# Kernel tuning notes

Hardware: AMD Instinct MI355X
Metric: run time of the kernel (lower is better)

## Reference

```python
import jax, jax.numpy as jnp
import numpy as np

# 47 skeleton edges (parent, child) from getSkeletalModelStructure()
EDGES = np.array([
    (0, 1), (1, 2), (2, 3), (3, 29), (1, 5), (5, 6), (6, 8), (8, 9), (8, 13),
    (8, 17), (8, 21), (8, 25), (9, 10), (10, 11), (11, 12), (13, 14), (14, 15),
    (15, 16), (17, 18), (18, 19), (19, 20), (21, 22), (22, 23), (23, 24),
    (25, 26), (26, 27), (27, 28), (29, 30), (29, 34), (29, 38), (29, 42),
    (29, 46), (30, 31), (31, 32), (32, 33), (34, 35), (35, 36), (36, 37),
    (38, 39), (39, 40), (40, 41), (42, 43), (43, 44), (44, 45), (46, 47),
    (47, 48), (48, 49)], dtype=np.int32)

N_JOINTS = 50
N_EDGES = 47


def _length_direct(pose):
    # pose: [B, T, 151]; drop counter channel, view as joints
    B, T = pose.shape[0], pose.shape[1]
    p = pose[..., :-1].reshape(B, T, N_JOINTS, 3)
    diff = p[:, :, EDGES[:, 0], :] - p[:, :, EDGES[:, 1], :]   # [B, T, 47, 3]
    length = jnp.linalg.norm(diff, axis=-1)                      # [B, T, 47]
    eps = jnp.finfo(pose.dtype).tiny
    direct = diff / (length + eps)[..., None]                    # [B, T, 47, 3]
    # torch stacks each [B,T,3] edge dir along dim=-1 -> [B,T,3,47], then reshapes
    directs = jnp.transpose(direct, (0, 1, 3, 2)).reshape(B, T, N_EDGES * 3)
    return length, directs


def setup_inputs() -> dict:
    key = jax.random.key(0)
    k1, k2 = jax.random.split(key)
    B, T, D = 128, 1024, 151
    preds = jax.random.normal(k1, (B, T, D), dtype=jnp.float32)
    targets = jax.random.normal(k2, (B, T, D), dtype=jnp.float32)
    return {"preds": preds, "targets": targets}


def reference(preds, targets):
    target_pad = 0.0
    mask = (targets != target_pad).astype(preds.dtype)           # [B, T, 151]
    preds_m = preds * mask
    targets_m = targets * mask
    _, preds_dir = _length_direct(preds_m)
    _, targets_dir = _length_direct(targets_m)
    preds_dir = preds_dir * mask[:, :, :N_EDGES * 3]
    targets_dir = targets_dir * mask[:, :, :N_EDGES * 3]
    # cfg: loss='l1' (mean abs), vel_loss='mse' (mean square), loss_scale=1.0
    l1 = jnp.mean(jnp.abs(preds_m - targets_m))
    vel_mse = jnp.mean(jnp.square(preds_dir - targets_dir))
    return l1 + 0.1 * vel_mse
```

## Files before the change

### kernel.cpp

```cpp
#include <hip/hip_runtime.h>


#define N_ROWS   (128 * 1024)
#define ROW      151
#define N_EDGES  47
#define GRID     8192
#define BLOCK    256
#define ROWS_PER_WAVE 4
#define WAVE_DWORDS (ROWS_PER_WAVE * ROW)
#define WAVE_F4 (WAVE_DWORDS / 4)
#define WAVE_TASKS (ROWS_PER_WAVE * N_EDGES)
#define S_STRIDE (ROW * 2)

#if __has_builtin(__builtin_amdgcn_rsqf)
__device__ __forceinline__ float fast_rsq(float x) { return __builtin_amdgcn_rsqf(x); }
#else
__device__ __forceinline__ float fast_rsq(float x) {
    float r; asm volatile("v_rsq_f32 %0, %1" : "=v"(r) : "v"(x)); return r;
}
#endif

#define E(p, c) ((unsigned)((p) * 6) | ((unsigned)((c) * 6) << 16))
__constant__ unsigned c_edge[N_EDGES] = {
    E(0,1),  E(1,2),  E(2,3),  E(3,29), E(1,5),  E(5,6),  E(6,8),  E(8,9),
    E(8,13), E(8,17), E(8,21), E(8,25), E(9,10), E(10,11),E(11,12),E(13,14),
    E(14,15),E(15,16),E(17,18),E(18,19),E(19,20),E(21,22),E(22,23),E(23,24),
    E(25,26),E(26,27),E(27,28),E(29,30),E(29,34),E(29,38),E(29,42),E(29,46),
    E(30,31),E(31,32),E(32,33),E(34,35),E(35,36),E(36,37),E(38,39),E(39,40),
    E(40,41),E(42,43),E(43,44),E(44,45),E(46,47),E(47,48),E(48,49)};

__global__ __launch_bounds__(BLOCK) void reg_loss_main(
        const float* __restrict__ preds, const float* __restrict__ targets,
        float* __restrict__ wsL, float* __restrict__ wsV) {
    __shared__ float S[4][ROWS_PER_WAVE * S_STRIDE];
    __shared__ float redL[4], redV[4];

    const int t = threadIdx.x;
    const int lane = t & 63;
    const int wave = t >> 6;
    float* __restrict__ Sw = S[wave];
    float4* __restrict__ S4 = (float4*)Sw;

    const long long base = ((long long)blockIdx.x * 4 + wave) * WAVE_DWORDS;
    const float4* __restrict__ p4 = (const float4*)(preds + base);
    const float4* __restrict__ t4 = (const float4*)(targets + base);

    int tr[3], te[3], tpi[3], tci[3];
#pragma unroll
    for (int k = 0; k < 3; ++k) {
        int task = lane + k * 64;
        int r = task / N_EDGES;
        int e = task - r * N_EDGES;
        if (task >= WAVE_TASKS) { r = 0; e = 0; }
        tr[k] = r; te[k] = e;
        unsigned pk = c_edge[e];
        tpi[k] = pk & 0xffff;
        tci[k] = pk >> 16;
    }

    float l1 = 0.f;
    float vel = 0.f;

#pragma unroll
    for (int k = 0; k < 3; ++k) {
        int i = lane + k * 64;
        if (i < WAVE_F4) {
            float4 pv = p4[i];
            float4 tv = t4[i];
            float4 pm;
            pm.x = (tv.x != 0.f) ? pv.x : 0.f;
            pm.y = (tv.y != 0.f) ? pv.y : 0.f;
            pm.z = (tv.z != 0.f) ? pv.z : 0.f;
            pm.w = (tv.w != 0.f) ? pv.w : 0.f;
            l1 += fabsf(pm.x - tv.x) + fabsf(pm.y - tv.y)
                + fabsf(pm.z - tv.z) + fabsf(pm.w - tv.w);
            float4 a = {pm.x, tv.x, pm.y, tv.y};
            float4 b = {pm.z, tv.z, pm.w, tv.w};
            S4[i * 2]     = a;
            S4[i * 2 + 1] = b;
        }
    }

#pragma unroll
    for (int k = 0; k < 3; ++k) {
        int task = lane + k * 64;
        if (task < WAVE_TASKS) {
            const float* __restrict__ R = Sw + tr[k] * S_STRIDE;
            int pi = tpi[k], ci = tci[k], e = te[k];
            float2 px = *(const float2*)(R + pi);
            float2 py = *(const float2*)(R + pi + 2);
            float2 pz = *(const float2*)(R + pi + 4);
            float2 cx = *(const float2*)(R + ci);
            float2 cy = *(const float2*)(R + ci + 2);
            float2 cz = *(const float2*)(R + ci + 4);
            float pdx = px.x - cx.x, pdy = py.x - cy.x, pdz = pz.x - cz.x;
            float tdx = px.y - cx.y, tdy = py.y - cy.y, tdz = pz.y - cz.y;
            float pd2 = pdx * pdx + pdy * pdy + pdz * pdz;
            float td2 = tdx * tdx + tdy * tdy + tdz * tdz;
            float pinv = (pd2 > 0.f) ? fast_rsq(pd2) : 0.f;
            float tinv = (td2 > 0.f) ? fast_rsq(td2) : 0.f;
            float dx = pdx * pinv - tdx * tinv;
            float dy = pdy * pinv - tdy * tinv;
            float dz = pdz * pinv - tdz * tinv;
            float m0 = (R[e * 2 + 1]        != 0.f) ? 1.f : 0.f;
            float m1 = (R[(47 + e) * 2 + 1] != 0.f) ? 1.f : 0.f;
            float m2 = (R[(94 + e) * 2 + 1] != 0.f) ? 1.f : 0.f;
            vel += m0 * dx * dx + m1 * dy * dy + m2 * dz * dz;
        }
    }

#pragma unroll
    for (int off = 32; off > 0; off >>= 1) {
        l1  += __shfl_down(l1, off);
        vel += __shfl_down(vel, off);
    }
    if (lane == 0) { redL[wave] = l1; redV[wave] = vel; }
    __syncthreads();
    if (t == 0) {
        wsL[blockIdx.x] = redL[0] + redL[1] + redL[2] + redL[3];
        wsV[blockIdx.x] = redV[0] + redV[1] + redV[2] + redV[3];
    }
}

__global__ __launch_bounds__(BLOCK) void reg_loss_finalize(
        const float* __restrict__ wsL, const float* __restrict__ wsV,
        float* __restrict__ out) {
    __shared__ double rl[4], rv[4];
    const int t = threadIdx.x;
    const int lane = t & 63;
    const int wave = t >> 6;
    double L = 0.0, V = 0.0;
    for (int k = t; k < GRID; k += BLOCK) { L += wsL[k]; V += wsV[k]; }
#pragma unroll
    for (int off = 32; off > 0; off >>= 1) {
        L += __shfl_down(L, off);
        V += __shfl_down(V, off);
    }
    if (lane == 0) { rl[wave] = L; rv[wave] = V; }
    __syncthreads();
    if (t == 0) {
        double Ls = rl[0] + rl[1] + rl[2] + rl[3];
        double Vs = rv[0] + rv[1] + rv[2] + rv[3];
        out[0] = (float)(Ls / ((double)N_ROWS * 151.0)
                       + 0.1 * (Vs / ((double)N_ROWS * 141.0)));
    }
}

extern "C" void kernel_launch(void* const* d_in, const int* in_sizes, int n_in,
                              void* d_out, int out_size, void* d_ws, size_t ws_size,
                              hipStream_t stream) {
    const float* preds   = (const float*)d_in[0];
    const float* targets = (const float*)d_in[1];
    float* wsL = (float*)d_ws;
    float* wsV = wsL + GRID;
    float* out = (float*)d_out;

    reg_loss_main<<<GRID, BLOCK, 0, stream>>>(preds, targets, wsL, wsV);
    reg_loss_finalize<<<1, BLOCK, 0, stream>>>(wsL, wsV, out);
}
```

Measured before the change: 180.7 us.

## Process eight row-chunks per wave with register double-buffered prefetch

Each wave now loops over eight 4-row chunks instead of handling a single chunk, and the grid shrinks from 8192 to 1024 blocks. The next chunk's global loads are issued into registers before the current chunk is masked, staged to LDS and reduced, so memory latency overlaps with compute. This amortizes the per-block reduction and launch cost and hides load latency. The trade-off is higher register pressure and fewer waves to saturate HBM bandwidth. The loop reuses the LDS buffer without any barrier, which is safe only because each wave stays in lockstep within its own region.

```diff
diff --git a/kernel.cpp b/kernel.cpp
--- a/kernel.cpp
+++ b/kernel.cpp
@@ -4,12 +4,13 @@
 #define N_ROWS   (128 * 1024)
 #define ROW      151
 #define N_EDGES  47
-#define GRID     8192
+#define GRID     1024
 #define BLOCK    256
-#define ROWS_PER_WAVE 4
-#define WAVE_DWORDS (ROWS_PER_WAVE * ROW)
-#define WAVE_F4 (WAVE_DWORDS / 4)
-#define WAVE_TASKS (ROWS_PER_WAVE * N_EDGES)
+#define WAVE_CHUNKS 8
+#define CHUNK_ROWS 4
+#define CHUNK_DWORDS (CHUNK_ROWS * ROW)
+#define CHUNK_F4 (CHUNK_DWORDS / 4)
+#define CHUNK_TASKS (CHUNK_ROWS * N_EDGES)
 #define S_STRIDE (ROW * 2)
 
 #if __has_builtin(__builtin_amdgcn_rsqf)
@@ -32,7 +33,7 @@
 __global__ __launch_bounds__(BLOCK) void reg_loss_main(
         const float* __restrict__ preds, const float* __restrict__ targets,
         float* __restrict__ wsL, float* __restrict__ wsV) {
-    __shared__ float S[4][ROWS_PER_WAVE * S_STRIDE];
+    __shared__ float S[4][CHUNK_ROWS * S_STRIDE];
     __shared__ float redL[4], redV[4];
 
     const int t = threadIdx.x;
@@ -41,71 +42,97 @@
     float* __restrict__ Sw = S[wave];
     float4* __restrict__ S4 = (float4*)Sw;
 
-    const long long base = ((long long)blockIdx.x * 4 + wave) * WAVE_DWORDS;
-    const float4* __restrict__ p4 = (const float4*)(preds + base);
-    const float4* __restrict__ t4 = (const float4*)(targets + base);
+    const long long wbase =
+        ((long long)blockIdx.x * 4 + wave) * (WAVE_CHUNKS * CHUNK_DWORDS);
+    const float4* __restrict__ p4 = (const float4*)(preds + wbase);
+    const float4* __restrict__ t4 = (const float4*)(targets + wbase);
 
-    int tr[3], te[3], tpi[3], tci[3];
+    int tRoff[3], tpi[3], tci[3], tm0[3];
+    bool tact[3];
 #pragma unroll
     for (int k = 0; k < 3; ++k) {
         int task = lane + k * 64;
+        tact[k] = task < CHUNK_TASKS;
         int r = task / N_EDGES;
         int e = task - r * N_EDGES;
-        if (task >= WAVE_TASKS) { r = 0; e = 0; }
-        tr[k] = r; te[k] = e;
+        if (!tact[k]) { r = 0; e = 0; }
+        tRoff[k] = r * S_STRIDE;
         unsigned pk = c_edge[e];
         tpi[k] = pk & 0xffff;
         tci[k] = pk >> 16;
+        tm0[k] = e * 2 + 1;
     }
 
     float l1 = 0.f;
     float vel = 0.f;
 
+    float4 Pp[3], Pt[3];
 #pragma unroll
     for (int k = 0; k < 3; ++k) {
         int i = lane + k * 64;
-        if (i < WAVE_F4) {
-            float4 pv = p4[i];
-            float4 tv = t4[i];
-            float4 pm;
-            pm.x = (tv.x != 0.f) ? pv.x : 0.f;
-            pm.y = (tv.y != 0.f) ? pv.y : 0.f;
-            pm.z = (tv.z != 0.f) ? pv.z : 0.f;
-            pm.w = (tv.w != 0.f) ? pv.w : 0.f;
-            l1 += fabsf(pm.x - tv.x) + fabsf(pm.y - tv.y)
-                + fabsf(pm.z - tv.z) + fabsf(pm.w - tv.w);
-            float4 a = {pm.x, tv.x, pm.y, tv.y};
-            float4 b = {pm.z, tv.z, pm.w, tv.w};
-            S4[i * 2]     = a;
-            S4[i * 2 + 1] = b;
-        }
+        if (i < CHUNK_F4) { Pp[k] = p4[i]; Pt[k] = t4[i]; }
     }
 
 #pragma unroll
-    for (int k = 0; k < 3; ++k) {
-        int task = lane + k * 64;
-        if (task < WAVE_TASKS) {
-            const float* __restrict__ R = Sw + tr[k] * S_STRIDE;
-            int pi = tpi[k], ci = tci[k], e = te[k];
-            float2 px = *(const float2*)(R + pi);
-            float2 py = *(const float2*)(R + pi + 2);
-            float2 pz = *(const float2*)(R + pi + 4);
-            float2 cx = *(const float2*)(R + ci);
-            float2 cy = *(const float2*)(R + ci + 2);
-            float2 cz = *(const float2*)(R + ci + 4);
-            float pdx = px.x - cx.x, pdy = py.x - cy.x, pdz = pz.x - cz.x;
-            float tdx = px.y - cx.y, tdy = py.y - cy.y, tdz = pz.y - cz.y;
-            float pd2 = pdx * pdx + pdy * pdy + pdz * pdz;
-            float td2 = tdx * tdx + tdy * tdy + tdz * tdz;
-            float pinv = (pd2 > 0.f) ? fast_rsq(pd2) : 0.f;
-            float tinv = (td2 > 0.f) ? fast_rsq(td2) : 0.f;
-            float dx = pdx * pinv - tdx * tinv;
-            float dy = pdy * pinv - tdy * tinv;
-            float dz = pdz * pinv - tdz * tinv;
-            float m0 = (R[e * 2 + 1]        != 0.f) ? 1.f : 0.f;
-            float m1 = (R[(47 + e) * 2 + 1] != 0.f) ? 1.f : 0.f;
-            float m2 = (R[(94 + e) * 2 + 1] != 0.f) ? 1.f : 0.f;
-            vel += m0 * dx * dx + m1 * dy * dy + m2 * dz * dz;
+    for (int c = 0; c < WAVE_CHUNKS; ++c) {
+        float4 Cp[3], Ct[3];
+#pragma unroll
+        for (int k = 0; k < 3; ++k) { Cp[k] = Pp[k]; Ct[k] = Pt[k]; }
+
+        if (c + 1 < WAVE_CHUNKS) {
+            const float4* np4 = p4 + (long long)(c + 1) * CHUNK_F4;
+            const float4* nt4 = t4 + (long long)(c + 1) * CHUNK_F4;
+#pragma unroll
+            for (int k = 0; k < 3; ++k) {
+                int i = lane + k * 64;
+                if (i < CHUNK_F4) { Pp[k] = np4[i]; Pt[k] = nt4[i]; }
+            }
+        }
+
+#pragma unroll
+        for (int k = 0; k < 3; ++k) {
+            int i = lane + k * 64;
+            if (i < CHUNK_F4) {
+                float4 pv = Cp[k], tv = Ct[k];
+                float4 pm;
+                pm.x = (tv.x != 0.f) ? pv.x : 0.f;
+                pm.y = (tv.y != 0.f) ? pv.y : 0.f;
+                pm.z = (tv.z != 0.f) ? pv.z : 0.f;
+                pm.w = (tv.w != 0.f) ? pv.w : 0.f;
+                l1 += fabsf(pm.x - tv.x) + fabsf(pm.y - tv.y)
+                    + fabsf(pm.z - tv.z) + fabsf(pm.w - tv.w);
+                float4 a = {pm.x, tv.x, pm.y, tv.y};
+                float4 b = {pm.z, tv.z, pm.w, tv.w};
+                S4[i * 2]     = a;
+                S4[i * 2 + 1] = b;
+            }
+        }
+
+#pragma unroll
+        for (int k = 0; k < 3; ++k) {
+            if (tact[k]) {
+                const float* __restrict__ R = Sw + tRoff[k];
+                int pi = tpi[k], ci = tci[k], me = tm0[k];
+                float2 px = *(const float2*)(R + pi);
+                float2 py = *(const float2*)(R + pi + 2);
+                float2 pz = *(const float2*)(R + pi + 4);
+                float2 cx = *(const float2*)(R + ci);
+                float2 cy = *(const float2*)(R + ci + 2);
+                float2 cz = *(const float2*)(R + ci + 4);
+                float pdx = px.x - cx.x, pdy = py.x - cy.x, pdz = pz.x - cz.x;
+                float tdx = px.y - cx.y, tdy = py.y - cy.y, tdz = pz.y - cz.y;
+                float pd2 = pdx * pdx + pdy * pdy + pdz * pdz;
+                float td2 = tdx * tdx + tdy * tdy + tdz * tdz;
+                float pinv = (pd2 > 0.f) ? fast_rsq(pd2) : 0.f;
+                float tinv = (td2 > 0.f) ? fast_rsq(td2) : 0.f;
+                float dx = pdx * pinv - tdx * tinv;
+                float dy = pdy * pinv - tdy * tinv;
+                float dz = pdz * pinv - tdz * tinv;
+                float m0 = (R[me]       != 0.f) ? 1.f : 0.f;
+                float m1 = (R[me + 94]  != 0.f) ? 1.f : 0.f;
+                float m2 = (R[me + 188] != 0.f) ? 1.f : 0.f;
+                vel += m0 * dx * dx + m1 * dy * dy + m2 * dz * dz;
+            }
         }
     }
 
```

New measurement: 179.8 us. Within noise of the previous version (-0.5%).

## Double-buffer per-wave chunks via global_load_lds DMA with fewer, longer-lived blocks

Applied to the files above, without the earlier changes.

Each wave now handles four 4-row chunks instead of one. Chunks are loaded straight into LDS through global_load_lds into two alternating buffers, and manual vmcnt/lgkmcnt waits overlap the next chunk's load with the current chunk's compute. The staged layout is no longer interleaved: preds and targets sit in separate LDS regions, and masking is recomputed from the targets during the edge pass. The grid shrinks 4x, so there are fewer waves to hide latency, and correctness depends on the hand-counted waitcnt values.

```diff
diff --git a/kernel.cpp b/kernel.cpp
--- a/kernel.cpp
+++ b/kernel.cpp
@@ -4,13 +4,13 @@
 #define N_ROWS   (128 * 1024)
 #define ROW      151
 #define N_EDGES  47
-#define GRID     8192
+#define GRID     2048
 #define BLOCK    256
-#define ROWS_PER_WAVE 4
-#define WAVE_DWORDS (ROWS_PER_WAVE * ROW)
-#define WAVE_F4 (WAVE_DWORDS / 4)
-#define WAVE_TASKS (ROWS_PER_WAVE * N_EDGES)
-#define S_STRIDE (ROW * 2)
+#define CHUNKS   4
+#define CHUNK_ROWS 4
+#define CHUNK_DW (CHUNK_ROWS * ROW)
+#define CHUNK_TASKS (CHUNK_ROWS * N_EDGES)
+#define BUF_DW (2 * CHUNK_DW)
 
 #if __has_builtin(__builtin_amdgcn_rsqf)
 __device__ __forceinline__ float fast_rsq(float x) { return __builtin_amdgcn_rsqf(x); }
@@ -20,7 +20,34 @@
 }
 #endif
 
-#define E(p, c) ((unsigned)((p) * 6) | ((unsigned)((c) * 6) << 16))
+template <int N>
+__device__ __forceinline__ void wait_vm() {
+    asm volatile("s_waitcnt vmcnt(%0)" :: "n"(N) : "memory");
+}
+__device__ __forceinline__ void wait_lgkm0() {
+    asm volatile("s_waitcnt lgkmcnt(0)" ::: "memory");
+}
+
+__device__ __forceinline__ void dma16(const float* g, float* l) {
+    __builtin_amdgcn_global_load_lds(
+        (const __attribute__((address_space(1))) unsigned*)g,
+        (__attribute__((address_space(3))) unsigned*)l, 16, 0, 0);
+}
+
+__device__ __forceinline__ void dma_chunk(const float* gp, const float* gt,
+                                          float* L, int lane) {
+    const int l4 = lane * 4;
+    dma16(gp + l4,        L);
+    dma16(gp + 256 + l4,  L + 256);
+    dma16(gt + l4,        L + CHUNK_DW);
+    dma16(gt + 256 + l4,  L + CHUNK_DW + 256);
+    if (lane < 23) {
+        dma16(gp + 512 + l4, L + 512);
+        dma16(gt + 512 + l4, L + CHUNK_DW + 512);
+    }
+}
+
+#define E(p, c) ((unsigned)((p) * 3) | ((unsigned)((c) * 3) << 16))
 __constant__ unsigned c_edge[N_EDGES] = {
     E(0,1),  E(1,2),  E(2,3),  E(3,29), E(1,5),  E(5,6),  E(6,8),  E(8,9),
     E(8,13), E(8,17), E(8,21), E(8,25), E(9,10), E(10,11),E(11,12),E(13,14),
@@ -29,72 +56,47 @@
     E(30,31),E(31,32),E(32,33),E(34,35),E(35,36),E(36,37),E(38,39),E(39,40),
     E(40,41),E(42,43),E(43,44),E(44,45),E(46,47),E(47,48),E(48,49)};
 
-__global__ __launch_bounds__(BLOCK) void reg_loss_main(
-        const float* __restrict__ preds, const float* __restrict__ targets,
-        float* __restrict__ wsL, float* __restrict__ wsV) {
-    __shared__ float S[4][ROWS_PER_WAVE * S_STRIDE];
-    __shared__ float redL[4], redV[4];
-
-    const int t = threadIdx.x;
-    const int lane = t & 63;
-    const int wave = t >> 6;
-    float* __restrict__ Sw = S[wave];
-    float4* __restrict__ S4 = (float4*)Sw;
-
-    const long long base = ((long long)blockIdx.x * 4 + wave) * WAVE_DWORDS;
-    const float4* __restrict__ p4 = (const float4*)(preds + base);
-    const float4* __restrict__ t4 = (const float4*)(targets + base);
-
-    int tr[3], te[3], tpi[3], tci[3];
-#pragma unroll
-    for (int k = 0; k < 3; ++k) {
-        int task = lane + k * 64;
-        int r = task / N_EDGES;
-        int e = task - r * N_EDGES;
-        if (task >= WAVE_TASKS) { r = 0; e = 0; }
-        tr[k] = r; te[k] = e;
-        unsigned pk = c_edge[e];
-        tpi[k] = pk & 0xffff;
-        tci[k] = pk >> 16;
-    }
-
-    float l1 = 0.f;
-    float vel = 0.f;
+struct TaskDesc { int act[3], roff[3], pi[3], ci[3], me[3]; };
+
+__device__ __forceinline__ void compute_chunk(
+        const float* __restrict__ B, int lane, const TaskDesc& td,
+        float& l1, float& vel) {
+    const float* __restrict__ Bp = B;
+    const float* __restrict__ Bt = B + CHUNK_DW;
 
 #pragma unroll
     for (int k = 0; k < 3; ++k) {
         int i = lane + k * 64;
-        if (i < WAVE_F4) {
-            float4 pv = p4[i];
-            float4 tv = t4[i];
-            float4 pm;
-            pm.x = (tv.x != 0.f) ? pv.x : 0.f;
-            pm.y = (tv.y != 0.f) ? pv.y : 0.f;
-            pm.z = (tv.z != 0.f) ? pv.z : 0.f;
-            pm.w = (tv.w != 0.f) ? pv.w : 0.f;
-            l1 += fabsf(pm.x - tv.x) + fabsf(pm.y - tv.y)
-                + fabsf(pm.z - tv.z) + fabsf(pm.w - tv.w);
-            float4 a = {pm.x, tv.x, pm.y, tv.y};
-            float4 b = {pm.z, tv.z, pm.w, tv.w};
-            S4[i * 2]     = a;
-            S4[i * 2 + 1] = b;
+        if (i < CHUNK_DW / 4) {
+            float4 pv = ((const float4*)Bp)[i];
+            float4 tv = ((const float4*)Bt)[i];
+            float a0 = (tv.x != 0.f) ? pv.x : 0.f;
+            float a1 = (tv.y != 0.f) ? pv.y : 0.f;
+            float a2 = (tv.z != 0.f) ? pv.z : 0.f;
+            float a3 = (tv.w != 0.f) ? pv.w : 0.f;
+            l1 += fabsf(a0 - tv.x) + fabsf(a1 - tv.y)
+                + fabsf(a2 - tv.z) + fabsf(a3 - tv.w);
         }
     }
 
 #pragma unroll
     for (int k = 0; k < 3; ++k) {
-        int task = lane + k * 64;
-        if (task < WAVE_TASKS) {
-            const float* __restrict__ R = Sw + tr[k] * S_STRIDE;
-            int pi = tpi[k], ci = tci[k], e = te[k];
-            float2 px = *(const float2*)(R + pi);
-            float2 py = *(const float2*)(R + pi + 2);
-            float2 pz = *(const float2*)(R + pi + 4);
-            float2 cx = *(const float2*)(R + ci);
-            float2 cy = *(const float2*)(R + ci + 2);
-            float2 cz = *(const float2*)(R + ci + 4);
-            float pdx = px.x - cx.x, pdy = py.x - cy.x, pdz = pz.x - cz.x;
-            float tdx = px.y - cx.y, tdy = py.y - cy.y, tdz = pz.y - cz.y;
+        if (td.act[k]) {
+            const float* __restrict__ Rp = Bp + td.roff[k];
+            const float* __restrict__ Rt = Bt + td.roff[k];
+            int pi = td.pi[k], ci = td.ci[k], me = td.me[k];
+            float tpx = Rt[pi], tpy = Rt[pi + 1], tpz = Rt[pi + 2];
+            float tcx = Rt[ci], tcy = Rt[ci + 1], tcz = Rt[ci + 2];
+            float ppx = Rp[pi], ppy = Rp[pi + 1], ppz = Rp[pi + 2];
+            float pcx = Rp[ci], pcy = Rp[ci + 1], pcz = Rp[ci + 2];
+            float apx = (tpx != 0.f) ? ppx : 0.f;
+            float apy = (tpy != 0.f) ? ppy : 0.f;
+            float apz = (tpz != 0.f) ? ppz : 0.f;
+            float acx = (tcx != 0.f) ? pcx : 0.f;
+            float acy = (tcy != 0.f) ? pcy : 0.f;
+            float acz = (tcz != 0.f) ? pcz : 0.f;
+            float pdx = apx - acx, pdy = apy - acy, pdz = apz - acz;
+            float tdx = tpx - tcx, tdy = tpy - tcy, tdz = tpz - tcz;
             float pd2 = pdx * pdx + pdy * pdy + pdz * pdz;
             float td2 = tdx * tdx + tdy * tdy + tdz * tdz;
             float pinv = (pd2 > 0.f) ? fast_rsq(pd2) : 0.f;
@@ -102,12 +104,66 @@
             float dx = pdx * pinv - tdx * tinv;
             float dy = pdy * pinv - tdy * tinv;
             float dz = pdz * pinv - tdz * tinv;
-            float m0 = (R[e * 2 + 1]        != 0.f) ? 1.f : 0.f;
-            float m1 = (R[(47 + e) * 2 + 1] != 0.f) ? 1.f : 0.f;
-            float m2 = (R[(94 + e) * 2 + 1] != 0.f) ? 1.f : 0.f;
+            float m0 = (Rt[me]      != 0.f) ? 1.f : 0.f;
+            float m1 = (Rt[me + 47] != 0.f) ? 1.f : 0.f;
+            float m2 = (Rt[me + 94] != 0.f) ? 1.f : 0.f;
             vel += m0 * dx * dx + m1 * dy * dy + m2 * dz * dz;
         }
     }
+}
+
+__global__ __launch_bounds__(BLOCK) void reg_loss_main(
+        const float* __restrict__ preds, const float* __restrict__ targets,
+        float* __restrict__ wsL, float* __restrict__ wsV) {
+    __shared__ float S[4][2][BUF_DW];
+    __shared__ float redL[4], redV[4];
+
+    const int t = threadIdx.x;
+    const int lane = t & 63;
+    const int wave = t >> 6;
+    float* B0 = &S[wave][0][0];
+    float* B1 = &S[wave][1][0];
+
+    const long long wb =
+        (long long)(blockIdx.x * 4 + wave) * (CHUNKS * CHUNK_DW);
+    const float* gp = preds + wb;
+    const float* gt = targets + wb;
+
+    TaskDesc td;
+#pragma unroll
+    for (int k = 0; k < 3; ++k) {
+        int task = lane + k * 64;
+        td.act[k] = task < CHUNK_TASKS;
+        int r = task / N_EDGES;
+        int e = task - r * N_EDGES;
+        if (!td.act[k]) { r = 0; e = 0; }
+        td.roff[k] = r * ROW;
+        unsigned pk = c_edge[e];
+        td.pi[k] = pk & 0xffff;
+        td.ci[k] = pk >> 16;
+        td.me[k] = e;
+    }
+
+    dma_chunk(gp,                gt,                B0, lane);
+    dma_chunk(gp + CHUNK_DW,     gt + CHUNK_DW,     B1, lane);
+
+    float l1 = 0.f, vel = 0.f;
+
+    wait_vm<6>();
+    compute_chunk(B0, lane, td, l1, vel);
+    wait_lgkm0();
+    dma_chunk(gp + 2 * CHUNK_DW, gt + 2 * CHUNK_DW, B0, lane);
+
+    wait_vm<6>();
+    compute_chunk(B1, lane, td, l1, vel);
+    wait_lgkm0();
+    dma_chunk(gp + 3 * CHUNK_DW, gt + 3 * CHUNK_DW, B1, lane);
+
+    wait_vm<6>();
+    compute_chunk(B0, lane, td, l1, vel);
+
+    wait_vm<0>();
+    compute_chunk(B1, lane, td, l1, vel);
 
 #pragma unroll
     for (int off = 32; off > 0; off >>= 1) {
```

Result: no change. 178.7 us (-1.1%).
